# Kernel optimization log

Measured on AMD Instinct MI355X. Metric: run time of the kernel, lower is better.

## Reference

```python
import jax, jax.numpy as jnp
import numpy as np

B, L, D, C = 8, 1024, 512, 4  # batch, maxlen, input_units(=output_unit), channel


def setup_inputs() -> dict:
    key = jax.random.key(0)
    ks = jax.random.split(key, 6)
    scale = 1.0 / np.sqrt(D)  # glorot-ish
    inputs = jax.random.normal(ks[0], (B, L, D), dtype=jnp.float32)
    pad_k = jnp.zeros((B, L, 1), dtype=jnp.float32)  # 0 = valid, -99999 = pad
    w_l = jax.random.normal(ks[1], (C, D, D), dtype=jnp.float32) * scale   # scalar_w per channel
    b_l = jnp.zeros((C,), dtype=jnp.float32)                                # scalar_b per channel
    w_v1 = jax.random.normal(ks[2], (C, D), dtype=jnp.float32) * scale     # vector_w1 [D,1] squeezed
    w_v2 = jax.random.normal(ks[3], (C, D, D), dtype=jnp.float32) * scale  # vector_w2
    b_v = jnp.zeros((C, D), dtype=jnp.float32)                              # vector_b [1,1,D] squeezed
    return {"inputs": inputs, "pad_k": pad_k, "w_l": w_l, "b_l": b_l,
            "w_v1": w_v1, "w_v2": w_v2, "b_v": b_v}


def reference(inputs, pad_k, w_l, b_l, w_v1, w_v2, b_v):
    # inputs: [B,L,D], pad_k: [B,L,1]. Dropout (mask_prob) is identity at inference.
    pad_k2 = (pad_k + 99999.0) / 99999.0              # [B,L,1], 1 at valid, 0 at pad
    pk = pad_k[:, None, :, 0]                          # [B,1,L]

    # --- scalar (pairwise bilinear) attention, all channels at once ---
    mat_l = jnp.einsum('bld,cde->bcle', inputs, w_l)   # [B,C,L,D]
    # M[b,c,i,j] = sum_d inputs[b,i,d] * mat_l[b,c,j,d] + b_l[c]
    M = jnp.einsum('bid,bcjd->bcij', inputs, mat_l) + b_l[None, :, None, None]
    A = jnp.tanh(M)                                    # [B,C,L,L]
    s = A.sum(axis=3)                                  # sum over j -> [B,C,L]
    a = jax.nn.softmax(pk + s, axis=-1)[..., None]     # softmax over L -> [B,C,L,1]

    # --- vector attention ---
    sb = jnp.tanh(jnp.einsum('bld,cde->bcle', inputs, w_v2) + b_v[None, :, None, :])  # [B,C,L,D]
    score_bar = jnp.einsum('bcld,cd->bcl', sb, w_v1) + pk                              # [B,C,L]
    a_bar = jax.nn.softmax(score_bar, axis=-1)                                         # [B,C,L]
    pooled = jnp.einsum('bcl,bld->bcd', a_bar, inputs)                                 # [B,C,D]

    # C_l = a_l * inputs + pooled(broadcast over L) * pad_k2
    C_l = a * inputs[:, None] + pooled[:, :, None, :] * pad_k2[:, None]                # [B,C,L,D]

    C_features = jnp.concatenate(
        [jnp.transpose(C_l, (0, 2, 3, 1)), inputs[..., None]], axis=-1)                # [B,L,D,C+1]
    return C_features, a, a_bar[..., None]
```

## Files before the change

### kernel.cpp

```cpp
#include <hip/hip_runtime.h>

#define BB 8
#define LL 1024
#define DD 512
#define CC 4

typedef unsigned short u16;
typedef unsigned int u32;
typedef __attribute__((ext_vector_type(8))) short bf16x8;
typedef __attribute__((ext_vector_type(4))) float f32x4;
typedef __attribute__((ext_vector_type(4))) unsigned short u16x4;
typedef __attribute__((ext_vector_type(4))) float float4v;

typedef __attribute__((address_space(1))) const u32 gu32;
typedef __attribute__((address_space(3))) u32 lu32;
typedef __attribute__((address_space(3))) u16 l16;

__device__ __forceinline__ void gload16(const void* g, void* l) {
  __builtin_amdgcn_global_load_lds((gu32*)g, (lu32*)l, 16, 0, 0);
}
__device__ __forceinline__ u32 lds_off(const u16* p) {
  return (u32)(uintptr_t)(l16*)p;
}

__device__ __forceinline__ u16 f2bf(float f) {
  unsigned u = __float_as_uint(f);
  u += 0x7FFF + ((u >> 16) & 1);
  return (u16)(u >> 16);
}
__device__ __forceinline__ float bf2f(u16 h) {
  return __uint_as_float(((unsigned)h) << 16);
}
__device__ __forceinline__ float fast_tanh(float x) {
  return 1.0f - 2.0f / (__expf(2.0f * x) + 1.0f);
}

__global__ __launch_bounds__(256) void k_split(const float4v* __restrict__ x,
                                               u16* __restrict__ hi, u16* __restrict__ lo) {
  int i = blockIdx.x * 256 + threadIdx.x;
  float4v v = x[i];
  u16x4 h, l;
#pragma unroll
  for (int k = 0; k < 4; ++k) {
    u16 hh = f2bf(v[k]);
    h[k] = hh;
    l[k] = f2bf(v[k] - bf2f(hh));
  }
  *(u16x4*)&hi[(size_t)i * 4] = h;
  *(u16x4*)&lo[(size_t)i * 4] = l;
}

__global__ __launch_bounds__(256) void k_tsplit(const float* __restrict__ w,
                                                u16* __restrict__ thi, u16* __restrict__ tlo) {
  __shared__ float t[32][33];
  int c = blockIdx.z;
  int tx = threadIdx.x;
  int ty = threadIdx.y;
  int e0 = blockIdx.x * 32, d0 = blockIdx.y * 32;
#pragma unroll
  for (int k = 0; k < 32; k += 8)
    t[ty + k][tx] = w[((size_t)c * DD + d0 + ty + k) * DD + e0 + tx];
  __syncthreads();
#pragma unroll
  for (int k = 0; k < 32; k += 8) {
    float v = t[tx][ty + k];
    size_t o = ((size_t)c * DD + e0 + ty + k) * DD + d0 + tx;
    u16 h = f2bf(v);
    thi[o] = h;
    if (tlo) tlo[o] = f2bf(v - bf2f(h));
  }
}

#define DSR(dst, addr, OFF) \
  asm volatile("ds_read_b128 %0, %1 offset:" #OFF : "=v"(dst) : "v"(addr))
#define LGKM(N) \
  do { __builtin_amdgcn_sched_barrier(0); \
       asm volatile("s_waitcnt lgkmcnt(" #N ")" ::: "memory"); \
       __builtin_amdgcn_sched_barrier(0); } while (0)

template<int NSEG, bool SPLIT>
__device__ __forceinline__ void gemm256(const u16* __restrict__ Ahi, const u16* __restrict__ Alo,
                                        const u16* __restrict__ Bhi, const u16* __restrict__ Blo,
                                        u16* lA, u16* lB, f32x4 (&acc)[8][4]) {
  const int tid = threadIdx.x;
  const int lane = tid & 63;
  const int wave = tid >> 6;
  const int wr = wave >> 2, wc = wave & 3;
  const int fr = lane & 15;
  const int fq = lane >> 4;
  const int srow = tid >> 2;
  const int xs = (tid & 3) ^ ((srow >> 1) & 3);
  const size_t soff = (size_t)srow * DD + (size_t)xs * 8;
  const int sidx = fq ^ ((fr >> 1) & 3);
  const u32 ra = lds_off(lA) + (u32)((wr * 128 + fr) * 64 + sidx * 16);
  const u32 rb = lds_off(lB) + (u32)((wc * 64 + fr) * 64 + sidx * 16);

  const int NT = NSEG * 16;

#define STAGE_PAIR(t, beo, half) do {                                         \
    const int seg_ = SPLIT ? ((t) >> 4) : 0;                                  \
    const int kp_ = ((t) & 15) * 32;                                          \
    const u16* As_ = (SPLIT && seg_ == 1) ? Alo : Ahi;                        \
    const u16* Bs_ = (SPLIT && seg_ == 2) ? Blo : Bhi;                        \
    gload16(As_ + soff + (size_t)(half) * 128 * DD + kp_,                     \
            lA + (beo) + tid * 8 + (half) * 4096);                            \
    gload16(Bs_ + soff + (size_t)(half) * 128 * DD + kp_,                     \
            lB + (beo) + tid * 8 + (half) * 4096);                            \
  } while (0)

#define MFMA2(m0, m1) do {                                                    \
    _Pragma("unroll")                                                         \
    for (int ni = 0; ni < 4; ++ni)                                            \
      acc[m0][ni] = __builtin_amdgcn_mfma_f32_16x16x32_bf16(                  \
          af[m0], bv[ni], acc[m0][ni], 0, 0, 0);                              \
    _Pragma("unroll")                                                         \
    for (int ni = 0; ni < 4; ++ni)                                            \
      acc[m1][ni] = __builtin_amdgcn_mfma_f32_16x16x32_bf16(                  \
          af[m1], bv[ni], acc[m1][ni], 0, 0, 0);                              \
  } while (0)

#define COMPUTE_PEEL(bo_) do {                                                \
    u32 aA_ = ra + (bo_), aB_ = rb + (bo_);                                   \
    bf16x8 af[8], bv[4];                                                      \
    DSR(bv[0], aB_, 0);    DSR(bv[1], aB_, 1024);                             \
    DSR(bv[2], aB_, 2048); DSR(bv[3], aB_, 3072);                             \
    DSR(af[0], aA_, 0);    DSR(af[1], aA_, 1024);                             \
    DSR(af[2], aA_, 2048); DSR(af[3], aA_, 3072);                             \
    LGKM(2);                                                                  \
    __builtin_amdgcn_s_setprio(1);                                            \
    MFMA2(0, 1);                                                              \
    DSR(af[4], aA_, 4096); DSR(af[5], aA_, 5120);                             \
    LGKM(2);                                                                  \
    MFMA2(2, 3);                                                              \
    DSR(af[6], aA_, 6144); DSR(af[7], aA_, 7168);                             \
    LGKM(2);                                                                  \
    MFMA2(4, 5);                                                              \
    LGKM(0);                                                                  \
    MFMA2(6, 7);                                                              \
    __builtin_amdgcn_s_setprio(0);                                            \
    __builtin_amdgcn_s_barrier();            \
  } while (0)

  STAGE_PAIR(0, 0, 0);      STAGE_PAIR(0, 0, 1);
  STAGE_PAIR(1, 8192, 0);   STAGE_PAIR(1, 8192, 1);
  int be = 16384;
  u32 bo = 0;
#pragma unroll 1
  for (int t = 0; t < NT - 2; ++t) {
    STAGE_PAIR(t + 2, be, 0);
    __builtin_amdgcn_sched_barrier(0);
    asm volatile("s_waitcnt vmcnt(6)" ::: "memory");
    __builtin_amdgcn_sched_barrier(0);
    __builtin_amdgcn_s_barrier();
    __builtin_amdgcn_sched_barrier(0);
    {
      u32 aA_ = ra + bo, aB_ = rb + bo;
      bf16x8 af[8], bv[4];
      DSR(bv[0], aB_, 0);    DSR(bv[1], aB_, 1024);
      DSR(bv[2], aB_, 2048); DSR(bv[3], aB_, 3072);
      DSR(af[0], aA_, 0);    DSR(af[1], aA_, 1024);
      DSR(af[2], aA_, 2048); DSR(af[3], aA_, 3072);
      LGKM(2);
      __builtin_amdgcn_s_setprio(1);
      MFMA2(0, 1);
      DSR(af[4], aA_, 4096); DSR(af[5], aA_, 5120);
      LGKM(2);
      MFMA2(2, 3);
      STAGE_PAIR(t + 2, be, 1);
      DSR(af[6], aA_, 6144); DSR(af[7], aA_, 7168);
      LGKM(2);
      MFMA2(4, 5);
      LGKM(0);
      MFMA2(6, 7);
      __builtin_amdgcn_s_setprio(0);
      __builtin_amdgcn_s_barrier();
    }
    be = (be == 16384) ? 0 : be + 8192;
    bo = (bo == 32768u) ? 0u : bo + 16384u;
  }
  __builtin_amdgcn_sched_barrier(0);
  asm volatile("s_waitcnt vmcnt(4)" ::: "memory");
  __builtin_amdgcn_sched_barrier(0);
  __builtin_amdgcn_s_barrier();
  __builtin_amdgcn_sched_barrier(0);
  COMPUTE_PEEL(bo);
  bo = (bo == 32768u) ? 0u : bo + 16384u;
  __builtin_amdgcn_sched_barrier(0);
  asm volatile("s_waitcnt vmcnt(0)" ::: "memory");
  __builtin_amdgcn_sched_barrier(0);
  __builtin_amdgcn_s_barrier();
  __builtin_amdgcn_sched_barrier(0);
  COMPUTE_PEEL(bo);
#undef STAGE_PAIR
#undef COMPUTE_PEEL
#undef MFMA2
}

__global__ __launch_bounds__(512, 2) void k_matl(const u16* __restrict__ Xhi, const u16* __restrict__ Xlo,
                                                 const u16* __restrict__ Whi, const u16* __restrict__ Wlo,
                                                 u16* __restrict__ mhi, u16* __restrict__ mlo) {
  __shared__ u16 lA[3 * 256 * 32];
  __shared__ u16 lB[3 * 256 * 32];
  int lin = blockIdx.x;
  int virt = (lin & 7) * 32 + (lin >> 3);
  int bc = virt >> 3, rem = virt & 7;
  int tm = rem >> 1, tn = rem & 1;
  int b = bc >> 2, c = bc & 3;
  const u16* Ahi = Xhi + (size_t)b * LL * DD + (size_t)tm * 256 * DD;
  const u16* Alo = Xlo + (size_t)b * LL * DD + (size_t)tm * 256 * DD;
  const u16* Bhi = Whi + (size_t)c * DD * DD + (size_t)tn * 256 * DD;
  const u16* Blo = Wlo + (size_t)c * DD * DD + (size_t)tn * 256 * DD;
  f32x4 acc[8][4];
#pragma unroll
  for (int mi = 0; mi < 8; ++mi)
#pragma unroll
    for (int ni = 0; ni < 4; ++ni) acc[mi][ni] = (f32x4){0.f, 0.f, 0.f, 0.f};
  gemm256<3, true>(Ahi, Alo, Bhi, Blo, lA, lB, acc);

  int lane = threadIdx.x & 63, wave = threadIdx.x >> 6;
  int wr = wave >> 2, wc = wave & 3;
  int rgrp = (lane >> 4) * 4, cidx = lane & 15;
#pragma unroll
  for (int mi = 0; mi < 8; ++mi)
#pragma unroll
    for (int ni = 0; ni < 4; ++ni) {
      int row = tm * 256 + wr * 128 + mi * 16 + rgrp;
      int col = tn * 256 + wc * 64 + ni * 16 + cidx;
#pragma unroll
      for (int j = 0; j < 4; ++j) {
        float v = acc[mi][ni][j];
        size_t o = ((size_t)bc * LL + row + j) * DD + col;
        u16 h = f2bf(v);
        mhi[o] = h;
        mlo[o] = f2bf(v - bf2f(h));
      }
    }
}

__global__ __launch_bounds__(512, 2) void k_s(const u16* __restrict__ Xhi, const u16* __restrict__ Xlo,
                                              const u16* __restrict__ mhi, const u16* __restrict__ mlo,
                                              const float* __restrict__ b_l, float* __restrict__ s_part) {
  __shared__ u16 lA[3 * 256 * 32];
  __shared__ u16 lB[3 * 256 * 32];
  int lin = blockIdx.x;
  int virt = (lin & 7) * 64 + (lin >> 3);
  int bc = virt >> 4, rem = virt & 15;
  int tm = rem >> 2, tn = rem & 3;
  int b = bc >> 2, c = bc & 3;
  const u16* Ahi = Xhi + (size_t)b * LL * DD + (size_t)tm * 256 * DD;
  const u16* Alo = Xlo + (size_t)b * LL * DD + (size_t)tm * 256 * DD;
  const u16* Bhi = mhi + (size_t)bc * LL * DD + (size_t)tn * 256 * DD;
  const u16* Blo = mlo + (size_t)bc * LL * DD + (size_t)tn * 256 * DD;
  f32x4 acc[8][4];
#pragma unroll
  for (int mi = 0; mi < 8; ++mi)
#pragma unroll
    for (int ni = 0; ni < 4; ++ni) acc[mi][ni] = (f32x4){0.f, 0.f, 0.f, 0.f};
  gemm256<3, true>(Ahi, Alo, Bhi, Blo, lA, lB, acc);

  int lane = threadIdx.x & 63, wave = threadIdx.x >> 6;
  int wr = wave >> 2, wc = wave & 3;
  float bl = b_l[c];
  float part[8][4];
#pragma unroll
  for (int mi = 0; mi < 8; ++mi)
#pragma unroll
    for (int j = 0; j < 4; ++j) part[mi][j] = 0.f;
#pragma unroll
  for (int mi = 0; mi < 8; ++mi)
#pragma unroll
    for (int ni = 0; ni < 4; ++ni)
#pragma unroll
      for (int j = 0; j < 4; ++j) part[mi][j] += fast_tanh(acc[mi][ni][j] + bl);
#pragma unroll
  for (int mi = 0; mi < 8; ++mi)
#pragma unroll
    for (int j = 0; j < 4; ++j) {
      float v = part[mi][j];
      v += __shfl_xor(v, 1, 64);
      v += __shfl_xor(v, 2, 64);
      v += __shfl_xor(v, 4, 64);
      v += __shfl_xor(v, 8, 64);
      part[mi][j] = v;
    }
  if ((lane & 15) == 0) {
    int slot = bc * 16 + tn * 4 + wc;
    int rg = (lane >> 4) * 4;
#pragma unroll
    for (int mi = 0; mi < 8; ++mi)
#pragma unroll
      for (int j = 0; j < 4; ++j) {
        int row = tm * 256 + wr * 128 + mi * 16 + rg + j;
        s_part[(size_t)slot * LL + row] = part[mi][j];
      }
  }
}

__global__ __launch_bounds__(512, 2) void k_sbar(const u16* __restrict__ Xhi, const u16* __restrict__ Wv2T,
                                                 const float* __restrict__ b_v, const float* __restrict__ w_v1,
                                                 float* __restrict__ sc_part) {
  __shared__ u16 lA[3 * 256 * 32];
  __shared__ u16 lB[3 * 256 * 32];
  int lin = blockIdx.x;
  int virt = (lin & 7) * 32 + (lin >> 3);
  int bc = virt >> 3, rem = virt & 7;
  int tm = rem >> 1, tn = rem & 1;
  int b = bc >> 2, c = bc & 3;
  const u16* Ahi = Xhi + (size_t)b * LL * DD + (size_t)tm * 256 * DD;
  const u16* Bhi = Wv2T + (size_t)c * DD * DD + (size_t)tn * 256 * DD;
  f32x4 acc[8][4];
#pragma unroll
  for (int mi = 0; mi < 8; ++mi)
#pragma unroll
    for (int ni = 0; ni < 4; ++ni) acc[mi][ni] = (f32x4){0.f, 0.f, 0.f, 0.f};
  gemm256<1, false>(Ahi, nullptr, Bhi, nullptr, lA, lB, acc);

  int lane = threadIdx.x & 63, wave = threadIdx.x >> 6;
  int wr = wave >> 2, wc = wave & 3;
  int cidx = lane & 15;
  float wv[4], bvv[4];
#pragma unroll
  for (int ni = 0; ni < 4; ++ni) {
    int col = tn * 256 + wc * 64 + ni * 16 + cidx;
    wv[ni] = w_v1[c * DD + col];
    bvv[ni] = b_v[c * DD + col];
  }
  float part[8][4];
#pragma unroll
  for (int mi = 0; mi < 8; ++mi)
#pragma unroll
    for (int j = 0; j < 4; ++j) part[mi][j] = 0.f;
#pragma unroll
  for (int mi = 0; mi < 8; ++mi)
#pragma unroll
    for (int ni = 0; ni < 4; ++ni)
#pragma unroll
      for (int j = 0; j < 4; ++j) part[mi][j] += fast_tanh(acc[mi][ni][j] + bvv[ni]) * wv[ni];
#pragma unroll
  for (int mi = 0; mi < 8; ++mi)
#pragma unroll
    for (int j = 0; j < 4; ++j) {
      float v = part[mi][j];
      v += __shfl_xor(v, 1, 64);
      v += __shfl_xor(v, 2, 64);
      v += __shfl_xor(v, 4, 64);
      v += __shfl_xor(v, 8, 64);
      part[mi][j] = v;
    }
  if ((lane & 15) == 0) {
    int slot = bc * 8 + tn * 4 + wc;
    int rg = (lane >> 4) * 4;
#pragma unroll
    for (int mi = 0; mi < 8; ++mi)
#pragma unroll
      for (int j = 0; j < 4; ++j) {
        int row = tm * 256 + wr * 128 + mi * 16 + rg + j;
        sc_part[(size_t)slot * LL + row] = part[mi][j];
      }
  }
}

__device__ __forceinline__ float blk_max(float v, float* red, int tid) {
#pragma unroll
  for (int m = 32; m >= 1; m >>= 1) v = fmaxf(v, __shfl_xor(v, m, 64));
  if ((tid & 63) == 0) red[tid >> 6] = v;
  __syncthreads();
  float r = red[0];
#pragma unroll
  for (int k = 1; k < 16; ++k) r = fmaxf(r, red[k]);
  __syncthreads();
  return r;
}
__device__ __forceinline__ float blk_sum(float v, float* red, int tid) {
#pragma unroll
  for (int m = 32; m >= 1; m >>= 1) v += __shfl_xor(v, m, 64);
  if ((tid & 63) == 0) red[tid >> 6] = v;
  __syncthreads();
  float r = red[0];
#pragma unroll
  for (int k = 1; k < 16; ++k) r += red[k];
  __syncthreads();
  return r;
}

__global__ __launch_bounds__(1024) void k_softmax(const float* __restrict__ s_part,
                                                  const float* __restrict__ sc_part,
                                                  const float* __restrict__ pad_k,
                                                  const float* __restrict__ X,
                                                  float* __restrict__ a_out,
                                                  float* __restrict__ abar_out,
                                                  float* __restrict__ pooled) {
  __shared__ float red[16];
  __shared__ float sm_abar[LL];
  __shared__ float pp[DD];
  int bc = blockIdx.x, b = bc >> 2;
  int i = threadIdx.x;
  float pk = pad_k[b * LL + i];

  float s = pk;
#pragma unroll
  for (int p = 0; p < 16; ++p) s += s_part[(size_t)(bc * 16 + p) * LL + i];
  float mx = blk_max(s, red, i);
  float e = expf(s - mx);
  float sum = blk_sum(e, red, i);
  float a = e / sum;
  a_out[bc * LL + i] = a;

  float sb = pk;
#pragma unroll
  for (int p = 0; p < 8; ++p) sb += sc_part[(size_t)(bc * 8 + p) * LL + i];
  float mx2 = blk_max(sb, red, i);
  float e2 = expf(sb - mx2);
  float sum2 = blk_sum(e2, red, i);
  float ab = e2 / sum2;
  abar_out[bc * LL + i] = ab;
  sm_abar[i] = ab;
  __syncthreads();

  {
    int d = i & (DD - 1), h = i >> 9;
    const float* xb = X + (size_t)b * LL * DD + (size_t)h * 512 * DD + d;
    const float* abp = sm_abar + h * 512;
    float a0 = 0.f, a1 = 0.f, a2 = 0.f, a3 = 0.f;
    for (int l = 0; l < 512; l += 4) {
      a0 += abp[l + 0] * xb[(size_t)(l + 0) * DD];
      a1 += abp[l + 1] * xb[(size_t)(l + 1) * DD];
      a2 += abp[l + 2] * xb[(size_t)(l + 2) * DD];
      a3 += abp[l + 3] * xb[(size_t)(l + 3) * DD];
    }
    float sv = (a0 + a1) + (a2 + a3);
    if (h == 1) pp[d] = sv;
    __syncthreads();
    if (h == 0) pooled[bc * DD + d] = sv + pp[d];
  }
}

__global__ __launch_bounds__(256) void k_assemble(const float* __restrict__ X,
                                                  const float* __restrict__ pad_k,
                                                  const float* __restrict__ a,
                                                  const float* __restrict__ pooled,
                                                  float* __restrict__ out) {
  __shared__ float buf[1280];
  int t = threadIdx.x;
  size_t idx = (size_t)blockIdx.x * 256 + t;
  int d = (int)(idx & (DD - 1));
  int bl = (int)(idx >> 9);
  int b = bl >> 10;
  int l = bl & (LL - 1);
  float x = X[idx];
  float pk2 = (pad_k[bl] + 99999.0f) * (1.0f / 99999.0f);
#pragma unroll
  for (int c = 0; c < 4; ++c) {
    float av = a[(size_t)(b * 4 + c) * LL + l];
    float pv = pooled[(size_t)(b * 4 + c) * DD + d];
    buf[t * 5 + c] = av * x + pv * pk2;
  }
  buf[t * 5 + 4] = x;
  __syncthreads();
  size_t base = (size_t)blockIdx.x * 1280;
#pragma unroll
  for (int k = 0; k < 5; ++k) out[base + k * 256 + t] = buf[k * 256 + t];
}

extern "C" void kernel_launch(void* const* d_in, const int* in_sizes, int n_in,
                              void* d_out, int out_size, void* d_ws, size_t ws_size,
                              hipStream_t stream) {
  (void)in_sizes; (void)n_in; (void)out_size;
  const float* X     = (const float*)d_in[0];
  const float* pad_k = (const float*)d_in[1];
  const float* w_l   = (const float*)d_in[2];
  const float* b_l   = (const float*)d_in[3];
  const float* w_v1  = (const float*)d_in[4];
  const float* w_v2  = (const float*)d_in[5];
  const float* b_v   = (const float*)d_in[6];
  float* out = (float*)d_out;

  char* wsp = (char*)d_ws;
  const size_t NEED = 26279936;
  bool small_ws = ws_size < NEED;
  u16* Xhi = (u16*)wsp;
  u16* Xlo = small_ws ? (u16*)((char*)d_out + 67108864)
                      : (u16*)(wsp + 8388608);
  size_t off = small_ws ? 8388608 : 16777216;
  u16* WlThi = (u16*)(wsp + off);  off += 2097152;
  u16* WlTlo = (u16*)(wsp + off);  off += 2097152;
  u16* Wv2T  = (u16*)(wsp + off);  off += 2097152;
  float* s_part  = (float*)(wsp + off); off += 2097152;
  float* sc_part = (float*)(wsp + off); off += 1048576;
  float* pooled  = (float*)(wsp + off); off += 65536;

  u16* mhi = (u16*)d_out;
  u16* mlo = (u16*)d_out + 16777216;

  float* a_out    = out + 20971520;
  float* abar_out = out + 21004288;

  k_split<<<4096, 256, 0, stream>>>((const float4v*)X, Xhi, Xlo);
  k_tsplit<<<dim3(16, 16, 4), dim3(32, 8), 0, stream>>>(w_l, WlThi, WlTlo);
  k_tsplit<<<dim3(16, 16, 4), dim3(32, 8), 0, stream>>>(w_v2, Wv2T, nullptr);

  k_matl<<<256, 512, 0, stream>>>(Xhi, Xlo, WlThi, WlTlo, mhi, mlo);
  k_s<<<512, 512, 0, stream>>>(Xhi, Xlo, mhi, mlo, b_l, s_part);
  k_sbar<<<256, 512, 0, stream>>>(Xhi, Wv2T, b_v, w_v1, sc_part);

  k_softmax<<<32, 1024, 0, stream>>>(s_part, sc_part, pad_k, X, a_out, abar_out, pooled);
  k_assemble<<<16384, 256, 0, stream>>>(X, pad_k, a_out, pooled, out);
}
```

Measured before the change: 240.7 us.

## Deepen GEMM LDS ring to four stages and drop per-iteration trailing barrier

Grows the shared GEMM pipeline in the three GEMM kernels from a 3-slot to a 4-slot LDS ring buffer and prefetches three k-tiles ahead instead of two. Because the slot being refilled was last read one iteration earlier, the barrier at the end of each iteration is removed, leaving one barrier per k-step. Wait counts and the epilogue peel are adjusted for the deeper pipeline. The cost is more LDS per block (128 KB instead of 96 KB), which still allows one 512-thread block per CU, and a longer prologue and epilogue.

```diff
diff --git a/kernel.cpp b/kernel.cpp
--- a/kernel.cpp
+++ b/kernel.cpp
@@ -76,6 +76,10 @@
 #define LGKM(N) \
   do { __builtin_amdgcn_sched_barrier(0); \
        asm volatile("s_waitcnt lgkmcnt(" #N ")" ::: "memory"); \
+       __builtin_amdgcn_sched_barrier(0); } while (0)
+#define VMCNT(N) \
+  do { __builtin_amdgcn_sched_barrier(0); \
+       asm volatile("s_waitcnt vmcnt(" #N ")" ::: "memory"); \
        __builtin_amdgcn_sched_barrier(0); } while (0)
 
 template<int NSEG, bool SPLIT>
@@ -97,16 +101,25 @@
 
   const int NT = NSEG * 16;
 
-#define STAGE_PAIR(t, beo, half) do {                                         \
-    const int seg_ = SPLIT ? ((t) >> 4) : 0;                                  \
-    const int kp_ = ((t) & 15) * 32;                                          \
+#define STAGE_TOP(T, beo) do {                                                \
+    const int seg_ = SPLIT ? ((T) >> 4) : 0;                                  \
+    const int kp_ = ((T) & 15) * 32;                                          \
     const u16* As_ = (SPLIT && seg_ == 1) ? Alo : Ahi;                        \
     const u16* Bs_ = (SPLIT && seg_ == 2) ? Blo : Bhi;                        \
-    gload16(As_ + soff + (size_t)(half) * 128 * DD + kp_,                     \
-            lA + (beo) + tid * 8 + (half) * 4096);                            \
-    gload16(Bs_ + soff + (size_t)(half) * 128 * DD + kp_,                     \
-            lB + (beo) + tid * 8 + (half) * 4096);                            \
+    gload16(As_ + soff + kp_, lA + (beo) + tid * 8);                          \
+    gload16(Bs_ + soff + kp_, lB + (beo) + tid * 8);                          \
   } while (0)
+
+#define STAGE_MID(T, beo) do {                                                \
+    const int seg_ = SPLIT ? ((T) >> 4) : 0;                                  \
+    const int kp_ = ((T) & 15) * 32;                                          \
+    const u16* As_ = (SPLIT && seg_ == 1) ? Alo : Ahi;                        \
+    const u16* Bs_ = (SPLIT && seg_ == 2) ? Blo : Bhi;                        \
+    gload16(As_ + soff + (size_t)128 * DD + kp_, lA + (beo) + tid * 8 + 4096); \
+    gload16(Bs_ + soff + (size_t)128 * DD + kp_, lB + (beo) + tid * 8 + 4096); \
+  } while (0)
+
+#define STAGE_ALL(T, beo) do { STAGE_TOP(T, beo); STAGE_MID(T, beo); } while (0)
 
 #define MFMA2(m0, m1) do {                                                    \
     _Pragma("unroll")                                                         \
@@ -138,21 +151,19 @@
     LGKM(0);                                                                  \
     MFMA2(6, 7);                                                              \
     __builtin_amdgcn_s_setprio(0);                                            \
-    __builtin_amdgcn_s_barrier();            \
   } while (0)
 
-  STAGE_PAIR(0, 0, 0);      STAGE_PAIR(0, 0, 1);
-  STAGE_PAIR(1, 8192, 0);   STAGE_PAIR(1, 8192, 1);
-  int be = 16384;
+  STAGE_ALL(0, 0);
+  STAGE_ALL(1, 8192);
+  STAGE_ALL(2, 16384);
+  u32 beN = 24576;
   u32 bo = 0;
 #pragma unroll 1
-  for (int t = 0; t < NT - 2; ++t) {
-    STAGE_PAIR(t + 2, be, 0);
-    __builtin_amdgcn_sched_barrier(0);
-    asm volatile("s_waitcnt vmcnt(6)" ::: "memory");
-    __builtin_amdgcn_sched_barrier(0);
+  for (int t = 0; t < NT - 3; ++t) {
+    VMCNT(8);
     __builtin_amdgcn_s_barrier();
     __builtin_amdgcn_sched_barrier(0);
+    STAGE_TOP(t + 3, beN);
     {
       u32 aA_ = ra + bo, aB_ = rb + bo;
       bf16x8 af[8], bv[4];
@@ -166,32 +177,34 @@
       DSR(af[4], aA_, 4096); DSR(af[5], aA_, 5120);
       LGKM(2);
       MFMA2(2, 3);
-      STAGE_PAIR(t + 2, be, 1);
+      STAGE_MID(t + 3, beN);
       DSR(af[6], aA_, 6144); DSR(af[7], aA_, 7168);
       LGKM(2);
       MFMA2(4, 5);
       LGKM(0);
       MFMA2(6, 7);
       __builtin_amdgcn_s_setprio(0);
-      __builtin_amdgcn_s_barrier();
     }
-    be = (be == 16384) ? 0 : be + 8192;
-    bo = (bo == 32768u) ? 0u : bo + 16384u;
-  }
-  __builtin_amdgcn_sched_barrier(0);
-  asm volatile("s_waitcnt vmcnt(4)" ::: "memory");
-  __builtin_amdgcn_sched_barrier(0);
+    beN = (beN + 8192) & 32767;
+    bo = (bo + 16384u) & 65535u;
+  }
+  VMCNT(8);
   __builtin_amdgcn_s_barrier();
   __builtin_amdgcn_sched_barrier(0);
   COMPUTE_PEEL(bo);
-  bo = (bo == 32768u) ? 0u : bo + 16384u;
-  __builtin_amdgcn_sched_barrier(0);
-  asm volatile("s_waitcnt vmcnt(0)" ::: "memory");
-  __builtin_amdgcn_sched_barrier(0);
+  bo = (bo + 16384u) & 65535u;
+  VMCNT(4);
   __builtin_amdgcn_s_barrier();
   __builtin_amdgcn_sched_barrier(0);
   COMPUTE_PEEL(bo);
-#undef STAGE_PAIR
+  bo = (bo + 16384u) & 65535u;
+  VMCNT(0);
+  __builtin_amdgcn_s_barrier();
+  __builtin_amdgcn_sched_barrier(0);
+  COMPUTE_PEEL(bo);
+#undef STAGE_TOP
+#undef STAGE_MID
+#undef STAGE_ALL
 #undef COMPUTE_PEEL
 #undef MFMA2
 }
@@ -199,8 +212,8 @@
 __global__ __launch_bounds__(512, 2) void k_matl(const u16* __restrict__ Xhi, const u16* __restrict__ Xlo,
                                                  const u16* __restrict__ Whi, const u16* __restrict__ Wlo,
                                                  u16* __restrict__ mhi, u16* __restrict__ mlo) {
-  __shared__ u16 lA[3 * 256 * 32];
-  __shared__ u16 lB[3 * 256 * 32];
+  __shared__ u16 lA[4 * 256 * 32];
+  __shared__ u16 lB[4 * 256 * 32];
   int lin = blockIdx.x;
   int virt = (lin & 7) * 32 + (lin >> 3);
   int bc = virt >> 3, rem = virt & 7;
@@ -240,8 +253,8 @@
 __global__ __launch_bounds__(512, 2) void k_s(const u16* __restrict__ Xhi, const u16* __restrict__ Xlo,
                                               const u16* __restrict__ mhi, const u16* __restrict__ mlo,
                                               const float* __restrict__ b_l, float* __restrict__ s_part) {
-  __shared__ u16 lA[3 * 256 * 32];
-  __shared__ u16 lB[3 * 256 * 32];
+  __shared__ u16 lA[4 * 256 * 32];
+  __shared__ u16 lB[4 * 256 * 32];
   int lin = blockIdx.x;
   int virt = (lin & 7) * 64 + (lin >> 3);
   int bc = virt >> 4, rem = virt & 15;
@@ -299,8 +312,8 @@
 __global__ __launch_bounds__(512, 2) void k_sbar(const u16* __restrict__ Xhi, const u16* __restrict__ Wv2T,
                                                  const float* __restrict__ b_v, const float* __restrict__ w_v1,
                                                  float* __restrict__ sc_part) {
-  __shared__ u16 lA[3 * 256 * 32];
-  __shared__ u16 lB[3 * 256 * 32];
+  __shared__ u16 lA[4 * 256 * 32];
+  __shared__ u16 lB[4 * 256 * 32];
   int lin = blockIdx.x;
   int virt = (lin & 7) * 32 + (lin >> 3);
   int bc = virt >> 3, rem = virt & 7;
```

Result: no change. 239.1 us (-0.7%).
